# Kernel optimization log

Measured on AMD Instinct MI355X. Metric: run time of the kernel, lower is better.

Reference implementation:

```python
import jax, jax.numpy as jnp
import numpy as np

B, T, D, FF, E = 4, 2048, 512, 2048, 8
TOP_K = 2
EPS = 0.01


def setup_inputs() -> dict:
    key = jax.random.key(0)
    ks = jax.random.split(key, 7)
    s = 0.02
    return {
        "x": jax.random.normal(ks[0], (B, T, D), dtype=jnp.float32),
        "Wg": jax.random.normal(ks[1], (D, E), dtype=jnp.float32) * s,
        "bg": jnp.zeros((E,), dtype=jnp.float32),
        "W1": jax.random.normal(ks[2], (E, D, FF), dtype=jnp.float32) * s,
        "b1": jnp.zeros((E, FF), dtype=jnp.float32),
        "W2": jax.random.normal(ks[3], (E, FF, D), dtype=jnp.float32) * s,
        "b2": jnp.zeros((E, D), dtype=jnp.float32),
    }


def reference(x, Wg, bg, W1, b1, W2, b2):
    b, t, d = x.shape
    e = Wg.shape[1]
    # Gating: softmax over experts, top-k selection, renormalize with eps.
    logits = jnp.einsum("btd,de->bte", x, Wg) + bg          # [B,T,E]
    gates = jax.nn.softmax(logits, axis=-1)
    vals, idx = jax.lax.top_k(gates, TOP_K)                  # [B,T,K]
    vals = vals / (jnp.sum(vals, axis=-1, keepdims=True) + EPS)
    # Per-token per-expert combine weight (scatter of top-k vals into E slots).
    w = jnp.sum(jax.nn.one_hot(idx, e, dtype=x.dtype) * vals[..., None], axis=-2)  # [B,T,E]
    w = w.reshape(-1, e)                                     # [N,E], N=B*T
    xf = x.reshape(-1, d)                                    # [N,D]
    # Per-expert FFN (Linear -> ReLU -> Linear); zero-weight tokens contribute 0,
    # matching the original's masked gather/scatter.
    h = jax.nn.relu(jnp.einsum("nd,edf->enf", xf, W1) + b1[:, None, :])  # [E,N,FF]
    y = jnp.einsum("enf,efd->end", h, W2) + b2[:, None, :]               # [E,N,D]
    out = jnp.einsum("ne,end->nd", w, y)                                 # [N,D]
    return out.reshape(b, t, d)
```

## Files before the change

### kernel.cpp

```cpp
#include <hip/hip_runtime.h>
#include <hip/hip_bf16.h>
#include <cstdint>

#define NTOK   8192
#define DDIM   512
#define FDIM   2048
#define NEXP   8
#define NSLOT  16384
#define MAXTILES 136

typedef __bf16 bf16;
typedef __bf16 bf16x8 __attribute__((ext_vector_type(8)));
typedef float  f32x4  __attribute__((ext_vector_type(4)));

typedef uint32_t __attribute__((address_space(1))) gu32;
typedef uint32_t __attribute__((address_space(3))) lu32;

__device__ __forceinline__ void gload16(const void* g, void* l) {
    __builtin_amdgcn_global_load_lds((const gu32*)(uintptr_t)g,
                                     (lu32*)(uintptr_t)l, 16, 0, 0);
}

__global__ __launch_bounds__(256)
void gating_kernel(const float* __restrict__ x, const float* __restrict__ Wg,
                   const float* __restrict__ bg, bf16* __restrict__ xb,
                   int* __restrict__ top_idx, float* __restrict__ top_w,
                   int* __restrict__ counts)
{
    __shared__ int cnt_s[NEXP];
    if (threadIdx.x < NEXP) cnt_s[threadIdx.x] = 0;
    __syncthreads();

    const int w = threadIdx.x >> 6;
    const int l = threadIdx.x & 63;
    const int gw = blockIdx.x * 4 + w;

    for (int n = gw; n < NTOK; n += 4096) {
        const float4* xp = (const float4*)(x + (size_t)n * DDIM + l * 8);
        float4 x0 = xp[0], x1 = xp[1];
        float xf[8] = {x0.x, x0.y, x0.z, x0.w, x1.x, x1.y, x1.z, x1.w};

        bf16x8 xv;
#pragma unroll
        for (int i = 0; i < 8; ++i) xv[i] = (bf16)xf[i];
        *(bf16x8*)(xb + (size_t)n * DDIM + l * 8) = xv;

        float acc[8] = {0.f,0.f,0.f,0.f,0.f,0.f,0.f,0.f};
#pragma unroll
        for (int i = 0; i < 8; ++i) {
            const float4* wp = (const float4*)(Wg + (size_t)(l * 8 + i) * NEXP);
            float4 wa = wp[0], wb = wp[1];
            acc[0] += xf[i] * wa.x; acc[1] += xf[i] * wa.y;
            acc[2] += xf[i] * wa.z; acc[3] += xf[i] * wa.w;
            acc[4] += xf[i] * wb.x; acc[5] += xf[i] * wb.y;
            acc[6] += xf[i] * wb.z; acc[7] += xf[i] * wb.w;
        }
#pragma unroll
        for (int m = 32; m >= 1; m >>= 1)
#pragma unroll
            for (int e = 0; e < 8; ++e)
                acc[e] += __shfl_xor(acc[e], m);

        if (l == 0) {
            float logit[8];
#pragma unroll
            for (int e = 0; e < 8; ++e) logit[e] = acc[e] + bg[e];
            float mx = logit[0];
#pragma unroll
            for (int e = 1; e < 8; ++e) mx = fmaxf(mx, logit[e]);
            float g[8], s = 0.f;
#pragma unroll
            for (int e = 0; e < 8; ++e) { g[e] = expf(logit[e] - mx); s += g[e]; }
            float inv = 1.f / s;
#pragma unroll
            for (int e = 0; e < 8; ++e) g[e] *= inv;
            int e0 = 0;
#pragma unroll
            for (int e = 1; e < 8; ++e) if (g[e] > g[e0]) e0 = e;
            int e1 = (e0 == 0) ? 1 : 0;
#pragma unroll
            for (int e = 0; e < 8; ++e) if (e != e0 && e != e1 && g[e] > g[e1]) e1 = e;
            float denom = g[e0] + g[e1] + 0.01f;
            top_idx[n * 2 + 0] = e0;
            top_idx[n * 2 + 1] = e1;
            top_w[n * 2 + 0] = g[e0] / denom;
            top_w[n * 2 + 1] = g[e1] / denom;
            atomicAdd(&cnt_s[e0], 1);
            atomicAdd(&cnt_s[e1], 1);
        }
    }
    __syncthreads();
    if (threadIdx.x < NEXP) atomicAdd(&counts[threadIdx.x], cnt_s[threadIdx.x]);
}

__global__ void scan_kernel(const int* __restrict__ counts, int* __restrict__ offsets,
                            int* __restrict__ tmap_e, int* __restrict__ tmap_rt,
                            int* __restrict__ ntiles, int* __restrict__ cursors)
{
    if (threadIdx.x == 0) {
        int off = 0;
        for (int e = 0; e < NEXP; ++e) { offsets[e] = off; off += counts[e]; cursors[e] = 0; }
        offsets[NEXP] = off;
        int t = 0;
        for (int e = 0; e < NEXP; ++e) {
            int nt = (counts[e] + 127) >> 7;
            for (int rt = 0; rt < nt; ++rt) { tmap_e[t] = e; tmap_rt[t] = rt; ++t; }
        }
        *ntiles = t;
    }
}

__global__ __launch_bounds__(256)
void scatter_kernel(const int* __restrict__ top_idx, const float* __restrict__ top_w,
                    const int* __restrict__ offsets, int* __restrict__ cursors,
                    int* __restrict__ slot_tok, float* __restrict__ slot_w,
                    int* __restrict__ pos)
{
    __shared__ int lcnt[NEXP];
    __shared__ int lbase[NEXP];
    const int t = threadIdx.x;
    if (t < NEXP) lcnt[t] = 0;
    __syncthreads();
    const int n = blockIdx.x * 256 + t;
    const int e0 = top_idx[n * 2 + 0];
    const int e1 = top_idx[n * 2 + 1];
    const int r0 = atomicAdd(&lcnt[e0], 1);
    const int r1 = atomicAdd(&lcnt[e1], 1);
    __syncthreads();
    if (t < NEXP) lbase[t] = atomicAdd(&cursors[t], lcnt[t]);
    __syncthreads();
    const int s0 = offsets[e0] + lbase[e0] + r0;
    const int s1 = offsets[e1] + lbase[e1] + r1;
    slot_tok[s0] = n; slot_w[s0] = top_w[n * 2 + 0]; pos[n * 2 + 0] = s0;
    slot_tok[s1] = n; slot_w[s1] = top_w[n * 2 + 1]; pos[n * 2 + 1] = s1;
}

__global__ __launch_bounds__(256)
void transpose_cvt(const float* __restrict__ src, bf16* __restrict__ dst, int R, int C)
{
    __shared__ bf16 tile[64][72];
    const size_t eo = (size_t)blockIdx.z * R * C;
    src += eo; dst += eo;
    const int c0 = blockIdx.x * 64, r0 = blockIdx.y * 64;
    const int tq = (threadIdx.x & 15) * 4;
    const int tr = threadIdx.x >> 4;
#pragma unroll
    for (int j = 0; j < 4; ++j) {
        const int r = tr + j * 16;
        float4 v = *(const float4*)(src + (size_t)(r0 + r) * C + c0 + tq);
        tile[tq + 0][r] = (bf16)v.x;
        tile[tq + 1][r] = (bf16)v.y;
        tile[tq + 2][r] = (bf16)v.z;
        tile[tq + 3][r] = (bf16)v.w;
    }
    __syncthreads();
    const int x8 = (threadIdx.x & 7) * 8;
    const int cr = threadIdx.x >> 3;
#pragma unroll
    for (int j = 0; j < 2; ++j) {
        const int c = cr + j * 32;
        *(bf16x8*)(dst + (size_t)(c0 + c) * R + r0 + x8) = *(const bf16x8*)&tile[c][x8];
    }
}

template<int KD, int ND, bool FIRST>
__global__ __launch_bounds__(512)
void moe_gemm(const bf16* __restrict__ Adata, const bf16* __restrict__ Bt,
              const float* __restrict__ bias, bf16* __restrict__ Out,
              const int* __restrict__ slot_tok, const int* __restrict__ offsets,
              const int* __restrict__ tmap_e, const int* __restrict__ tmap_rt,
              const int* __restrict__ ntiles)
{
    constexpr int NX  = ND / 128;
    constexpr int NWG = NX * MAXTILES;
    constexpr int Q   = NWG / 8;
    constexpr int NT  = KD / 32;

    const int orig = blockIdx.y * NX + blockIdx.x;
    const int work = (orig & 7) * Q + (orig >> 3);
    const int wy   = work / NX;
    const int wx   = work - wy * NX;
    if (wy >= *ntiles) return;

    const int e    = tmap_e[wy];
    const int rt   = tmap_rt[wy];
    const int row0 = offsets[e] + rt * 128;
    const int rowEnd = offsets[e + 1];
    const int nb   = wx * 128;

    __shared__ __align__(16) bf16 As[2 * 128 * 32];
    __shared__ __align__(16) bf16 Bs[2 * 128 * 32];

    const int t = threadIdx.x;
    const int w = t >> 6, l = t & 63;
    const int wm = w >> 1, wn = w & 1;

    const int rA   = w * 16 + (l >> 2);
    const int colb = (((l & 3) ^ ((l >> 3) & 3)) * 8);

    int srow = row0 + rA; if (srow >= NSLOT) srow = NSLOT - 1;
    const bf16* aSrc;
    if (FIRST) aSrc = Adata + (size_t)slot_tok[srow] * KD + colb;
    else       aSrc = Adata + (size_t)srow * KD + colb;
    const bf16* bSrc = Bt + ((size_t)e * ND + nb + rA) * KD + colb;

    const int offW = w * 512;

    f32x4 acc[2][4] = {};
    const int lr = l & 15;
    const int lks = (((l >> 4) ^ ((lr >> 1) & 3)) * 8);

    auto STAGE = [&](int buf, int k0) {
        gload16(aSrc + k0, As + buf * 4096 + offW);
        gload16(bSrc + k0, Bs + buf * 4096 + offW);
    };
    auto COMPUTE = [&](int buf) {
        const bf16* ab = As + buf * 4096;
        const bf16* bb = Bs + buf * 4096;
        bf16x8 aF[2], bF[4];
#pragma unroll
        for (int mi = 0; mi < 2; ++mi)
            aF[mi] = *(const bf16x8*)(ab + (wm * 32 + mi * 16 + lr) * 32 + lks);
#pragma unroll
        for (int nj = 0; nj < 4; ++nj)
            bF[nj] = *(const bf16x8*)(bb + (wn * 64 + nj * 16 + lr) * 32 + lks);
#pragma unroll
        for (int mi = 0; mi < 2; ++mi)
#pragma unroll
            for (int nj = 0; nj < 4; ++nj)
                acc[mi][nj] = __builtin_amdgcn_mfma_f32_16x16x32_bf16(
                    aF[mi], bF[nj], acc[mi][nj], 0, 0, 0);
    };

    STAGE(0, 0);
    __syncthreads();

    int buf = 0;
    for (int t2 = 0; t2 < NT - 1; ++t2) {
        STAGE(buf ^ 1, (t2 + 1) * 32);
        COMPUTE(buf);
        __syncthreads();
        buf ^= 1;
    }
    COMPUTE(buf);

    const int rowW = row0 + wm * 32;
    const int colW = nb + wn * 64;
#pragma unroll
    for (int mi = 0; mi < 2; ++mi) {
#pragma unroll
        for (int nj = 0; nj < 4; ++nj) {
#pragma unroll
            for (int r = 0; r < 4; ++r) {
                int row = rowW + mi * 16 + (l >> 4) * 4 + r;
                int col = colW + nj * 16 + lr;
                if (row < rowEnd) {
                    float v = acc[mi][nj][r] + bias[e * ND + col];
                    if (FIRST) v = fmaxf(v, 0.f);
                    Out[(size_t)row * ND + col] = (bf16)v;
                }
            }
        }
    }
}

__global__ __launch_bounds__(256)
void combine_kernel(const bf16* __restrict__ Yg, const int* __restrict__ pos,
                    const float* __restrict__ slot_w, float* __restrict__ out)
{
    const int idx = blockIdx.x * 256 + threadIdx.x;
    const int n  = idx >> 6;
    const int d8 = (idx & 63) * 8;
    const int s0 = pos[n * 2 + 0], s1 = pos[n * 2 + 1];
    const float w0 = slot_w[s0], w1 = slot_w[s1];
    bf16x8 a = *(const bf16x8*)(Yg + (size_t)s0 * DDIM + d8);
    bf16x8 b = *(const bf16x8*)(Yg + (size_t)s1 * DDIM + d8);
    float o[8];
#pragma unroll
    for (int j = 0; j < 8; ++j)
        o[j] = w0 * (float)a[j] + w1 * (float)b[j];
    float* op = out + (size_t)n * DDIM + d8;
    *(float4*)(op + 0) = make_float4(o[0], o[1], o[2], o[3]);
    *(float4*)(op + 4) = make_float4(o[4], o[5], o[6], o[7]);
}

extern "C" void kernel_launch(void* const* d_in, const int* in_sizes, int n_in,
                              void* d_out, int out_size, void* d_ws, size_t ws_size,
                              hipStream_t stream)
{
    (void)in_sizes; (void)n_in;
    const float* x  = (const float*)d_in[0];
    const float* Wg = (const float*)d_in[1];
    const float* bg = (const float*)d_in[2];
    const float* W1 = (const float*)d_in[3];
    const float* b1 = (const float*)d_in[4];
    const float* W2 = (const float*)d_in[5];
    const float* b2 = (const float*)d_in[6];
    float* out = (float*)d_out;

    uint8_t* ws = (uint8_t*)d_ws;
    size_t off = 0;
    auto alloc = [&](size_t bytes) -> void* {
        void* p = ws + off;
        off = (off + bytes + 255) & ~(size_t)255;
        return p;
    };
    bf16*  xb      = (bf16*)alloc((size_t)NTOK * DDIM * 2);
    bf16*  w1t     = (bf16*)alloc((size_t)NEXP * FDIM * DDIM * 2);
    bf16*  w2t     = (bf16*)alloc((size_t)NEXP * DDIM * FDIM * 2);
    bf16*  Hg      = (bf16*)alloc((size_t)NSLOT * FDIM * 2);
    bf16*  Yg      = (bf16*)alloc((size_t)NSLOT * DDIM * 2);
    int*   counts  = (int*)alloc(NEXP * 4);
    int*   cursors = (int*)alloc(NEXP * 4);
    int*   offsets = (int*)alloc((NEXP + 1) * 4);
    int*   ntiles  = (int*)alloc(4);
    int*   tmap_e  = (int*)alloc(MAXTILES * 4);
    int*   tmap_rt = (int*)alloc(MAXTILES * 4);
    int*   top_idx = (int*)alloc((size_t)NTOK * 2 * 4);
    float* top_w   = (float*)alloc((size_t)NTOK * 2 * 4);
    int*   pos     = (int*)alloc((size_t)NTOK * 2 * 4);
    int*   slot_tok= (int*)alloc((size_t)NSLOT * 4);
    float* slot_w  = (float*)alloc((size_t)NSLOT * 4);

    if (ws_size < off) {
        hipMemsetAsync(d_out, 0, (size_t)out_size * 4, stream);
        return;
    }

    hipMemsetAsync(counts, 0, NEXP * 4, stream);

    gating_kernel<<<1024, 256, 0, stream>>>(x, Wg, bg, xb, top_idx, top_w, counts);
    scan_kernel<<<1, 64, 0, stream>>>(counts, offsets, tmap_e, tmap_rt, ntiles, cursors);
    scatter_kernel<<<NTOK / 256, 256, 0, stream>>>(top_idx, top_w, offsets, cursors,
                                                   slot_tok, slot_w, pos);
    transpose_cvt<<<dim3(FDIM / 64, DDIM / 64, NEXP), 256, 0, stream>>>(W1, w1t, DDIM, FDIM);
    transpose_cvt<<<dim3(DDIM / 64, FDIM / 64, NEXP), 256, 0, stream>>>(W2, w2t, FDIM, DDIM);

    moe_gemm<DDIM, FDIM, true><<<dim3(FDIM / 128, MAXTILES), 512, 0, stream>>>(
        xb, w1t, b1, Hg, slot_tok, offsets, tmap_e, tmap_rt, ntiles);
    moe_gemm<FDIM, DDIM, false><<<dim3(DDIM / 128, MAXTILES), 512, 0, stream>>>(
        Hg, w2t, b2, Yg, slot_tok, offsets, tmap_e, tmap_rt, ntiles);

    combine_kernel<<<(NTOK * DDIM / 8) / 256, 256, 0, stream>>>(Yg, pos, slot_w, out);
}
```

Baseline: 176.1 us.

## Merge gating with weight transposes; fuse combine into second GEMM via atomics

```diff
diff --git a/kernel.cpp b/kernel.cpp
--- a/kernel.cpp
+++ b/kernel.cpp
@@ -22,75 +22,114 @@
 }
 
 __global__ __launch_bounds__(256)
-void gating_kernel(const float* __restrict__ x, const float* __restrict__ Wg,
-                   const float* __restrict__ bg, bf16* __restrict__ xb,
-                   int* __restrict__ top_idx, float* __restrict__ top_w,
-                   int* __restrict__ counts)
-{
-    __shared__ int cnt_s[NEXP];
-    if (threadIdx.x < NEXP) cnt_s[threadIdx.x] = 0;
-    __syncthreads();
-
-    const int w = threadIdx.x >> 6;
-    const int l = threadIdx.x & 63;
-    const int gw = blockIdx.x * 4 + w;
-
-    for (int n = gw; n < NTOK; n += 4096) {
-        const float4* xp = (const float4*)(x + (size_t)n * DDIM + l * 8);
-        float4 x0 = xp[0], x1 = xp[1];
-        float xf[8] = {x0.x, x0.y, x0.z, x0.w, x1.x, x1.y, x1.z, x1.w};
-
-        bf16x8 xv;
-#pragma unroll
-        for (int i = 0; i < 8; ++i) xv[i] = (bf16)xf[i];
-        *(bf16x8*)(xb + (size_t)n * DDIM + l * 8) = xv;
-
-        float acc[8] = {0.f,0.f,0.f,0.f,0.f,0.f,0.f,0.f};
-#pragma unroll
-        for (int i = 0; i < 8; ++i) {
-            const float4* wp = (const float4*)(Wg + (size_t)(l * 8 + i) * NEXP);
-            float4 wa = wp[0], wb = wp[1];
-            acc[0] += xf[i] * wa.x; acc[1] += xf[i] * wa.y;
-            acc[2] += xf[i] * wa.z; acc[3] += xf[i] * wa.w;
-            acc[4] += xf[i] * wb.x; acc[5] += xf[i] * wb.y;
-            acc[6] += xf[i] * wb.z; acc[7] += xf[i] * wb.w;
-        }
-#pragma unroll
-        for (int m = 32; m >= 1; m >>= 1)
-#pragma unroll
-            for (int e = 0; e < 8; ++e)
-                acc[e] += __shfl_xor(acc[e], m);
-
-        if (l == 0) {
-            float logit[8];
-#pragma unroll
-            for (int e = 0; e < 8; ++e) logit[e] = acc[e] + bg[e];
-            float mx = logit[0];
-#pragma unroll
-            for (int e = 1; e < 8; ++e) mx = fmaxf(mx, logit[e]);
-            float g[8], s = 0.f;
-#pragma unroll
-            for (int e = 0; e < 8; ++e) { g[e] = expf(logit[e] - mx); s += g[e]; }
-            float inv = 1.f / s;
-#pragma unroll
-            for (int e = 0; e < 8; ++e) g[e] *= inv;
-            int e0 = 0;
-#pragma unroll
-            for (int e = 1; e < 8; ++e) if (g[e] > g[e0]) e0 = e;
-            int e1 = (e0 == 0) ? 1 : 0;
-#pragma unroll
-            for (int e = 0; e < 8; ++e) if (e != e0 && e != e1 && g[e] > g[e1]) e1 = e;
-            float denom = g[e0] + g[e1] + 0.01f;
-            top_idx[n * 2 + 0] = e0;
-            top_idx[n * 2 + 1] = e1;
-            top_w[n * 2 + 0] = g[e0] / denom;
-            top_w[n * 2 + 1] = g[e1] / denom;
-            atomicAdd(&cnt_s[e0], 1);
-            atomicAdd(&cnt_s[e1], 1);
-        }
-    }
-    __syncthreads();
-    if (threadIdx.x < NEXP) atomicAdd(&counts[threadIdx.x], cnt_s[threadIdx.x]);
+void prep_kernel(const float* __restrict__ x, const float* __restrict__ Wg,
+                 const float* __restrict__ bg, bf16* __restrict__ xb,
+                 int* __restrict__ top_idx, float* __restrict__ top_w,
+                 int* __restrict__ counts,
+                 const float* __restrict__ W1, bf16* __restrict__ w1t,
+                 const float* __restrict__ W2, bf16* __restrict__ w2t)
+{
+    const int bid = blockIdx.x;
+    if (bid < 1024) {
+        __shared__ int cnt_s[NEXP];
+        if (threadIdx.x < NEXP) cnt_s[threadIdx.x] = 0;
+        __syncthreads();
+
+        const int w = threadIdx.x >> 6;
+        const int l = threadIdx.x & 63;
+        const int gw = bid * 4 + w;
+
+        for (int n = gw; n < NTOK; n += 4096) {
+            const float4* xp = (const float4*)(x + (size_t)n * DDIM + l * 8);
+            float4 x0 = xp[0], x1 = xp[1];
+            float xf[8] = {x0.x, x0.y, x0.z, x0.w, x1.x, x1.y, x1.z, x1.w};
+
+            bf16x8 xv;
+#pragma unroll
+            for (int i = 0; i < 8; ++i) xv[i] = (bf16)xf[i];
+            *(bf16x8*)(xb + (size_t)n * DDIM + l * 8) = xv;
+
+            float acc[8] = {0.f,0.f,0.f,0.f,0.f,0.f,0.f,0.f};
+#pragma unroll
+            for (int i = 0; i < 8; ++i) {
+                const float4* wp = (const float4*)(Wg + (size_t)(l * 8 + i) * NEXP);
+                float4 wa = wp[0], wb = wp[1];
+                acc[0] += xf[i] * wa.x; acc[1] += xf[i] * wa.y;
+                acc[2] += xf[i] * wa.z; acc[3] += xf[i] * wa.w;
+                acc[4] += xf[i] * wb.x; acc[5] += xf[i] * wb.y;
+                acc[6] += xf[i] * wb.z; acc[7] += xf[i] * wb.w;
+            }
+#pragma unroll
+            for (int m = 32; m >= 1; m >>= 1)
+#pragma unroll
+                for (int e = 0; e < 8; ++e)
+                    acc[e] += __shfl_xor(acc[e], m);
+
+            if (l == 0) {
+                float logit[8];
+#pragma unroll
+                for (int e = 0; e < 8; ++e) logit[e] = acc[e] + bg[e];
+                float mx = logit[0];
+#pragma unroll
+                for (int e = 1; e < 8; ++e) mx = fmaxf(mx, logit[e]);
+                float g[8], s = 0.f;
+#pragma unroll
+                for (int e = 0; e < 8; ++e) { g[e] = expf(logit[e] - mx); s += g[e]; }
+                float inv = 1.f / s;
+#pragma unroll
+                for (int e = 0; e < 8; ++e) g[e] *= inv;
+                int e0 = 0;
+#pragma unroll
+                for (int e = 1; e < 8; ++e) if (g[e] > g[e0]) e0 = e;
+                int e1 = (e0 == 0) ? 1 : 0;
+#pragma unroll
+                for (int e = 0; e < 8; ++e) if (e != e0 && e != e1 && g[e] > g[e1]) e1 = e;
+                float denom = g[e0] + g[e1] + 0.01f;
+                top_idx[n * 2 + 0] = e0;
+                top_idx[n * 2 + 1] = e1;
+                top_w[n * 2 + 0] = g[e0] / denom;
+                top_w[n * 2 + 1] = g[e1] / denom;
+                atomicAdd(&cnt_s[e0], 1);
+                atomicAdd(&cnt_s[e1], 1);
+            }
+        }
+        __syncthreads();
+        if (threadIdx.x < NEXP) atomicAdd(&counts[threadIdx.x], cnt_s[threadIdx.x]);
+    } else {
+        const float* src; bf16* dst; int R, C, bx, by, bz;
+        if (bid < 3072) {
+            const int idx = bid - 1024;
+            src = W1; dst = w1t; R = DDIM; C = FDIM;
+            bx = idx & 31; by = (idx >> 5) & 7; bz = idx >> 8;
+        } else {
+            const int idx = bid - 3072;
+            src = W2; dst = w2t; R = FDIM; C = DDIM;
+            bx = idx & 7; by = (idx >> 3) & 31; bz = idx >> 8;
+        }
+        __shared__ bf16 tile[64][72];
+        const size_t eo = (size_t)bz * R * C;
+        src += eo; dst += eo;
+        const int c0 = bx * 64, r0 = by * 64;
+        const int tq = (threadIdx.x & 15) * 4;
+        const int tr = threadIdx.x >> 4;
+#pragma unroll
+        for (int j = 0; j < 4; ++j) {
+            const int r = tr + j * 16;
+            float4 v = *(const float4*)(src + (size_t)(r0 + r) * C + c0 + tq);
+            tile[tq + 0][r] = (bf16)v.x;
+            tile[tq + 1][r] = (bf16)v.y;
+            tile[tq + 2][r] = (bf16)v.z;
+            tile[tq + 3][r] = (bf16)v.w;
+        }
+        __syncthreads();
+        const int x8 = (threadIdx.x & 7) * 8;
+        const int cr = threadIdx.x >> 3;
+#pragma unroll
+        for (int j = 0; j < 2; ++j) {
+            const int c = cr + j * 32;
+            *(bf16x8*)(dst + (size_t)(c0 + c) * R + r0 + x8) = *(const bf16x8*)&tile[c][x8];
+        }
+    }
 }
 
 __global__ void scan_kernel(const int* __restrict__ counts, int* __restrict__ offsets,
@@ -135,38 +174,11 @@
     slot_tok[s1] = n; slot_w[s1] = top_w[n * 2 + 1]; pos[n * 2 + 1] = s1;
 }
 
-__global__ __launch_bounds__(256)
-void transpose_cvt(const float* __restrict__ src, bf16* __restrict__ dst, int R, int C)
-{
-    __shared__ bf16 tile[64][72];
-    const size_t eo = (size_t)blockIdx.z * R * C;
-    src += eo; dst += eo;
-    const int c0 = blockIdx.x * 64, r0 = blockIdx.y * 64;
-    const int tq = (threadIdx.x & 15) * 4;
-    const int tr = threadIdx.x >> 4;
-#pragma unroll
-    for (int j = 0; j < 4; ++j) {
-        const int r = tr + j * 16;
-        float4 v = *(const float4*)(src + (size_t)(r0 + r) * C + c0 + tq);
-        tile[tq + 0][r] = (bf16)v.x;
-        tile[tq + 1][r] = (bf16)v.y;
-        tile[tq + 2][r] = (bf16)v.z;
-        tile[tq + 3][r] = (bf16)v.w;
-    }
-    __syncthreads();
-    const int x8 = (threadIdx.x & 7) * 8;
-    const int cr = threadIdx.x >> 3;
-#pragma unroll
-    for (int j = 0; j < 2; ++j) {
-        const int c = cr + j * 32;
-        *(bf16x8*)(dst + (size_t)(c0 + c) * R + r0 + x8) = *(const bf16x8*)&tile[c][x8];
-    }
-}
-
 template<int KD, int ND, bool FIRST>
 __global__ __launch_bounds__(512)
 void moe_gemm(const bf16* __restrict__ Adata, const bf16* __restrict__ Bt,
               const float* __restrict__ bias, bf16* __restrict__ Out,
+              float* __restrict__ out_f, const float* __restrict__ slot_w,
               const int* __restrict__ slot_tok, const int* __restrict__ offsets,
               const int* __restrict__ tmap_e, const int* __restrict__ tmap_rt,
               const int* __restrict__ ntiles)
@@ -256,32 +268,16 @@
                 int col = colW + nj * 16 + lr;
                 if (row < rowEnd) {
                     float v = acc[mi][nj][r] + bias[e * ND + col];
-                    if (FIRST) v = fmaxf(v, 0.f);
-                    Out[(size_t)row * ND + col] = (bf16)v;
+                    if (FIRST) {
+                        Out[(size_t)row * ND + col] = (bf16)fmaxf(v, 0.f);
+                    } else {
+                        atomicAdd(out_f + (size_t)slot_tok[row] * ND + col,
+                                  slot_w[row] * v);
+                    }
                 }
             }
         }
     }
-}
-
-__global__ __launch_bounds__(256)
-void combine_kernel(const bf16* __restrict__ Yg, const int* __restrict__ pos,
-                    const float* __restrict__ slot_w, float* __restrict__ out)
-{
-    const int idx = blockIdx.x * 256 + threadIdx.x;
-    const int n  = idx >> 6;
-    const int d8 = (idx & 63) * 8;
-    const int s0 = pos[n * 2 + 0], s1 = pos[n * 2 + 1];
-    const float w0 = slot_w[s0], w1 = slot_w[s1];
-    bf16x8 a = *(const bf16x8*)(Yg + (size_t)s0 * DDIM + d8);
-    bf16x8 b = *(const bf16x8*)(Yg + (size_t)s1 * DDIM + d8);
-    float o[8];
-#pragma unroll
-    for (int j = 0; j < 8; ++j)
-        o[j] = w0 * (float)a[j] + w1 * (float)b[j];
-    float* op = out + (size_t)n * DDIM + d8;
-    *(float4*)(op + 0) = make_float4(o[0], o[1], o[2], o[3]);
-    *(float4*)(op + 4) = make_float4(o[4], o[5], o[6], o[7]);
 }
 
 extern "C" void kernel_launch(void* const* d_in, const int* in_sizes, int n_in,
@@ -309,7 +305,6 @@
     bf16*  w1t     = (bf16*)alloc((size_t)NEXP * FDIM * DDIM * 2);
     bf16*  w2t     = (bf16*)alloc((size_t)NEXP * DDIM * FDIM * 2);
     bf16*  Hg      = (bf16*)alloc((size_t)NSLOT * FDIM * 2);
-    bf16*  Yg      = (bf16*)alloc((size_t)NSLOT * DDIM * 2);
     int*   counts  = (int*)alloc(NEXP * 4);
     int*   cursors = (int*)alloc(NEXP * 4);
     int*   offsets = (int*)alloc((NEXP + 1) * 4);
@@ -328,18 +323,16 @@
     }
 
     hipMemsetAsync(counts, 0, NEXP * 4, stream);
-
-    gating_kernel<<<1024, 256, 0, stream>>>(x, Wg, bg, xb, top_idx, top_w, counts);
+    hipMemsetAsync(out, 0, (size_t)out_size * 4, stream);
+
+    prep_kernel<<<5120, 256, 0, stream>>>(x, Wg, bg, xb, top_idx, top_w, counts,
+                                          W1, w1t, W2, w2t);
     scan_kernel<<<1, 64, 0, stream>>>(counts, offsets, tmap_e, tmap_rt, ntiles, cursors);
     scatter_kernel<<<NTOK / 256, 256, 0, stream>>>(top_idx, top_w, offsets, cursors,
                                                    slot_tok, slot_w, pos);
-    transpose_cvt<<<dim3(FDIM / 64, DDIM / 64, NEXP), 256, 0, stream>>>(W1, w1t, DDIM, FDIM);
-    transpose_cvt<<<dim3(DDIM / 64, FDIM / 64, NEXP), 256, 0, stream>>>(W2, w2t, FDIM, DDIM);
 
     moe_gemm<DDIM, FDIM, true><<<dim3(FDIM / 128, MAXTILES), 512, 0, stream>>>(
-        xb, w1t, b1, Hg, slot_tok, offsets, tmap_e, tmap_rt, ntiles);
+        xb, w1t, b1, Hg, nullptr, slot_w, slot_tok, offsets, tmap_e, tmap_rt, ntiles);
     moe_gemm<FDIM, DDIM, false><<<dim3(DDIM / 128, MAXTILES), 512, 0, stream>>>(
-        Hg, w2t, b2, Yg, slot_tok, offsets, tmap_e, tmap_rt, ntiles);
-
-    combine_kernel<<<(NTOK * DDIM / 8) / 256, 256, 0, stream>>>(Yg, pos, slot_w, out);
-}
+        Hg, w2t, b2, nullptr, out, slot_w, slot_tok, offsets, tmap_e, tmap_rt, ntiles);
+}
```

Result: no change. 177.9 us (+1.1%).
